# Kernel optimization log

Measured on AMD Instinct MI355X. Metric: run time of the kernel, lower is better.

The kernel has to match this reference:

```python
import jax, jax.numpy as jnp
import numpy as np

WS = 8        # window_size
OWIN = 12     # overlap_win_size = int(8*0.5)+8
PAD = 2       # (OWIN - WS)//2
HEADS = 4
DH = 16
INNER = HEADS * DH  # 64
DIM = 64


def _unfold(x, ws=WS, owin=OWIN, pad=PAD):
    # torch nn.Unfold(kernel=(owin,owin), stride=ws, padding=pad):
    # output [b, C*owin*owin, L] with channel ordering (c, kh, kw), L row-major over windows
    b, c, h, w = x.shape
    xp = jnp.pad(x, ((0, 0), (0, 0), (pad, pad), (pad, pad)))
    nH, nW = h // ws, w // ws
    ri = (jnp.arange(nH) * ws)[:, None] + jnp.arange(owin)[None, :]  # [nH, owin]
    ci = (jnp.arange(nW) * ws)[:, None] + jnp.arange(owin)[None, :]  # [nW, owin]
    p = xp[:, :, ri, :]          # [b, c, nH, owin, Wp]
    p = p[:, :, :, :, ci]        # [b, c, nH, owin, nW, owin]
    p = p.transpose(0, 1, 3, 5, 2, 4)  # [b, c, kh, kw, nH, nW]
    return p.reshape(b, c * owin * owin, nH * nW)


def setup_inputs() -> dict:
    key = jax.random.key(0)
    k1, k2, k3 = jax.random.split(key, 3)
    x = jax.random.normal(k1, (1, DIM, 64, 64), jnp.float32)
    w_qkv = jax.random.normal(k2, (3 * INNER, DIM), jnp.float32) * 0.05  # 1x1 conv, no bias
    w_out = jax.random.normal(k3, (DIM, INNER), jnp.float32) * 0.05     # 1x1 conv, no bias
    ln_w = jnp.ones((DIM,), jnp.float32)
    return {"x": x, "w_qkv": w_qkv, "w_out": w_out, "ln_w": ln_w}


def reference(x, w_qkv, w_out, ln_w):
    b, c, h, w = x.shape
    # BiasFree LayerNorm over channel dim (no mean subtraction)
    xc = x.transpose(0, 2, 3, 1)                       # b h w c
    var = jnp.var(xc, axis=-1, keepdims=True)
    xn = (xc / jnp.sqrt(var + 1e-5) * ln_w).transpose(0, 3, 1, 2)
    # qkv 1x1 conv
    qkv = jnp.einsum('bchw,oc->bohw', xn, w_qkv)
    qs, ks, vs = jnp.split(qkv, 3, axis=1)
    # queries: all h*w positions
    qs = qs.transpose(0, 2, 3, 1).reshape(b, h * w, HEADS, DH).transpose(0, 2, 1, 3)  # b heads N dh
    # keys/values: overlapping unfolded windows (faithful to torch reshape order)
    kk = _unfold(ks).reshape(b, INNER, -1).reshape(b, HEADS, -1, DH)  # b heads M dh
    vv = _unfold(vs).reshape(b, INNER, -1).reshape(b, HEADS, -1, DH)
    # rel_pos and fixed_mask are all-zero tensors in the source -> no-op bias
    attn = jnp.einsum('bhnd,bhmd->bhnm', qs, kk) * (DH ** -0.5)
    attn = jax.nn.softmax(attn, axis=-1)
    out = jnp.einsum('bhnm,bhmd->bhnd', attn, vv)
    out = out.transpose(0, 2, 1, 3).reshape(b, h, w, INNER).transpose(0, 3, 1, 2)
    return jnp.einsum('bchw,oc->bohw', out, w_out)
```

## Files before the change

### kernel.cpp

```cpp
#include <hip/hip_runtime.h>
#include <math.h>

#define PIX 4096
typedef unsigned short ushort_t;
typedef unsigned int uint_t;
typedef __attribute__((ext_vector_type(8))) short bf16x8;
typedef __attribute__((ext_vector_type(16))) float f32x16;

#define OFF_APART 524288
#define OFF_USHORT 2752512
#define U_QH 0
#define U_QL 262144
#define U_KF 524288
#define U_VF 1703936

#define QSCALE 0.36067376022224087f

#if defined(__has_builtin)
#if __has_builtin(__builtin_amdgcn_exp2f)
#define EXP2F(x) __builtin_amdgcn_exp2f(x)
#endif
#if __has_builtin(__builtin_amdgcn_perm)
#define PKHI16(u1, u0) __builtin_amdgcn_perm((u1), (u0), 0x07060302u)
#endif
#endif
#ifndef EXP2F
#define EXP2F(x) exp2f(x)
#endif
#ifndef PKHI16
#define PKHI16(u1, u0) (((u0) >> 16) | ((u1) & 0xFFFF0000u))
#endif

__device__ __forceinline__ void split_trunc(float x, ushort_t& hb, ushort_t& lb) {
    uint_t u = __float_as_uint(x);
    uint_t t = u & 0xFFFF0000u;
    float lo = x - __uint_as_float(t);
    hb = (ushort_t)(u >> 16);
    lb = (ushort_t)(__float_as_uint(lo) >> 16);
}

__device__ __forceinline__ void split8(const float* v, bf16x8& H, bf16x8& L) {
    union { uint_t u[4]; bf16x8 b; } hh, ll;
    #pragma unroll
    for (int j = 0; j < 4; ++j) {
        uint_t u0 = __float_as_uint(v[2 * j]), u1 = __float_as_uint(v[2 * j + 1]);
        hh.u[j] = PKHI16(u1, u0);
        float l0 = v[2 * j]     - __uint_as_float(u0 & 0xFFFF0000u);
        float l1 = v[2 * j + 1] - __uint_as_float(u1 & 0xFFFF0000u);
        ll.u[j] = PKHI16(__float_as_uint(l1), __float_as_uint(l0));
    }
    H = hh.b; L = ll.b;
}

__global__ __launch_bounds__(256)
void k_nq(const float* __restrict__ x, const float* __restrict__ w_qkv,
          const float* __restrict__ ln_w, float* __restrict__ qkvB,
          ushort_t* __restrict__ QH, ushort_t* __restrict__ QL)
{
    __shared__ float xs[64 * 32];
    __shared__ float red[2][8][32];
    __shared__ float rstd_s[32];
    __shared__ float lw[64];
    __shared__ ushort_t xh[32 * 64];
    __shared__ ushort_t xl[32 * 64];

    const int tid = threadIdx.x;
    const int px = tid & 31, cg = tid >> 5;
    const int pbase = ((int)blockIdx.x >> 1) * 32;
    const int ohalf = blockIdx.x & 1;

    if (tid < 64) lw[tid] = ln_w[tid];
    float s = 0.f, s2 = 0.f;
    #pragma unroll
    for (int cl = 0; cl < 8; ++cl) {
        int c = cg * 8 + cl;
        float v = x[c * PIX + pbase + px];
        xs[c * 32 + px] = v;
        s += v; s2 = fmaf(v, v, s2);
    }
    red[0][cg][px] = s; red[1][cg][px] = s2;
    __syncthreads();
    if (tid < 32) {
        float a = 0.f, b = 0.f;
        #pragma unroll
        for (int gidx = 0; gidx < 8; ++gidx) { a += red[0][gidx][tid]; b += red[1][gidx][tid]; }
        float mean = a * 0.015625f;
        float var  = fmaf(-mean, mean, b * 0.015625f);
        rstd_s[tid] = 1.0f / sqrtf(var + 1e-5f);
    }
    __syncthreads();
    {
        float vals[8];
        const float r = rstd_s[px];
        #pragma unroll
        for (int cl = 0; cl < 8; ++cl) {
            int c = cg * 8 + cl;
            vals[cl] = xs[c * 32 + px] * r * lw[c];
        }
        bf16x8 H, L; split8(vals, H, L);
        const int g = cg ^ (px & 7);
        *(bf16x8*)&xh[px * 64 + g * 8] = H;
        *(bf16x8*)&xl[px * 64 + g * 8] = L;
    }
    __syncthreads();

    const int w = tid >> 6;
    if (w >= 3) return;
    const int l = tid & 63, col = l & 31, rl = l >> 5;
    const int obase = ohalf * 96 + w * 32;

    bf16x8 wh[4], wl[4], xhf[4], xlf[4];
    const float* wrow = w_qkv + (obase + col) * 64;
    #pragma unroll
    for (int s4 = 0; s4 < 4; ++s4) {
        float tmp[8];
        *(float4*)&tmp[0] = *(const float4*)&wrow[s4 * 16 + rl * 8];
        *(float4*)&tmp[4] = *(const float4*)&wrow[s4 * 16 + rl * 8 + 4];
        split8(tmp, wh[s4], wl[s4]);
        const int g = (s4 * 2 + rl) ^ (col & 7);
        xhf[s4] = *(const bf16x8*)&xh[col * 64 + g * 8];
        xlf[s4] = *(const bf16x8*)&xl[col * 64 + g * 8];
    }
    f32x16 acc = {0,0,0,0,0,0,0,0,0,0,0,0,0,0,0,0};
    #pragma unroll
    for (int s4 = 0; s4 < 4; ++s4) {
        acc = __builtin_amdgcn_mfma_f32_32x32x16_bf16(wh[s4], xhf[s4], acc, 0, 0, 0);
        acc = __builtin_amdgcn_mfma_f32_32x32x16_bf16(wl[s4], xhf[s4], acc, 0, 0, 0);
        acc = __builtin_amdgcn_mfma_f32_32x32x16_bf16(wh[s4], xlf[s4], acc, 0, 0, 0);
    }
    const int gpx = pbase + col;
    #pragma unroll
    for (int j = 0; j < 16; ++j) {
        const int o = obase + (j & 3) + 8 * (j >> 2) + 4 * rl;
        if (o < 64) {
            float qv = acc[j] * QSCALE;
            ushort_t hb, lb; split_trunc(qv, hb, lb);
            const int a = ((o >> 4) * PIX + gpx) * 16 + (o & 15);
            QH[a] = hb; QL[a] = lb;
        } else {
            qkvB[(o - 64) * PIX + gpx] = acc[j];
        }
    }
}

__global__ __launch_bounds__(256)
void k_prep_kv(const float* __restrict__ qkvB,
               ushort_t* __restrict__ KF, ushort_t* __restrict__ VF)
{
    const int t = blockIdx.x * 256 + threadIdx.x;
    if (t < 589824) {
        int h = t / 147456; int r = t - h * 147456;
        int i = r >> 9; int r2 = r & 511;
        int l = r2 >> 3, j = r2 & 7;
        int col = l & 31, rl = l >> 5;
        int m = i * 32 + col;
        int d = rl * 8 + j;
        int cc = m / 576;  int r3 = m - cc * 576;
        int orr = r3 / 48; int r4 = r3 - orr * 48;
        int oc = r4 >> 2, wg = r4 & 3;
        int row  = wg * 16 + (d >> 3) * 8 + orr - 2;
        int colp = (d & 7) * 8 + oc - 2;
        bool ok = ((unsigned)row < 64u) && ((unsigned)colp < 64u);
        float v = ok ? qkvB[(h * 16 + cc) * PIX + row * 64 + colp] : 0.f;
        ushort_t hb, lb; split_trunc(v, hb, lb);
        int base = (h * 288 + i) * 1024 + l * 8 + j;
        KF[base] = hb; KF[base + 512] = lb;
    } else {
        int t2 = t - 589824;
        int h = t2 / 147456; int r = t2 - h * 147456;
        int i = r >> 9; int r2 = r & 511;
        int half = r2 >> 8; int r3 = r2 & 255;
        int rl = r3 >> 7; int colD = (r3 >> 3) & 15; int j2 = r3 & 7;
        int m = i * 32 + half * 16 + rl * 4 + (j2 & 3) + 8 * (j2 >> 2);
        int d = colD;
        int cc = m / 576;  int r4 = m - cc * 576;
        int orr = r4 / 48; int r5 = r4 - orr * 48;
        int oc = r5 >> 2, wg = r5 & 3;
        int row  = wg * 16 + (d >> 3) * 8 + orr - 2;
        int colp = (d & 7) * 8 + oc - 2;
        bool ok = ((unsigned)row < 64u) && ((unsigned)colp < 64u);
        float v = ok ? qkvB[(64 + h * 16 + cc) * PIX + row * 64 + colp] : 0.f;
        uint_t u = __float_as_uint(v);
        VF[(h * 288 + i) * 512 + half * 256 + (rl * 16 + colD) * 8 + j2] = (ushort_t)(u >> 16);
    }
}

__global__ __launch_bounds__(256)
void k_attn(const ushort_t* __restrict__ QH, const ushort_t* __restrict__ QL,
            const ushort_t* __restrict__ KF, const ushort_t* __restrict__ VF,
            float* __restrict__ APart)
{
    const int tid = threadIdx.x;
    const int w   = tid >> 6;
    const int l   = tid & 63;
    const int col = l & 31;
    const int rl  = l >> 5;

    const int bid  = blockIdx.x;
    const int x    = bid & 7;
    const int h    = x >> 1;
    const int tile = bid >> 3;
    const int ks   = (x & 1) * 4 + w;
    const int qbase = tile * 32;

    const bf16x8 qh = *(const bf16x8*)&QH[((h << 12) + qbase + col) * 16 + rl * 8];
    const bf16x8 ql = *(const bf16x8*)&QL[((h << 12) + qbase + col) * 16 + rl * 8];

    f32x16 acc = {0,0,0,0,0,0,0,0,0,0,0,0,0,0,0,0};
    const f32x16 zero = {0,0,0,0,0,0,0,0,0,0,0,0,0,0,0,0};

    union { uint_t u[4]; bf16x8 b; } vconst;
    const uint_t cfill = (col == 16) ? 0x3F803F80u : 0u;
    vconst.u[0] = cfill; vconst.u[1] = cfill; vconst.u[2] = cfill; vconst.u[3] = cfill;

    const ushort_t* kb = KF + (h * 288 + ks * 36) * 1024;
    const ushort_t* vb = VF + (h * 288 + ks * 36) * 512;

    bf16x8 kh = *(const bf16x8*)&kb[l * 8];
    bf16x8 kl = *(const bf16x8*)&kb[512 + l * 8];
    bf16x8 v0 = vconst.b, v1 = vconst.b;
    if (col < 16) {
        v0 = *(const bf16x8*)&vb[(rl * 16 + col) * 8];
        v1 = *(const bf16x8*)&vb[256 + (rl * 16 + col) * 8];
    }

    for (int i = 0; i < 36; ++i) {
        const bf16x8 ckh = kh, ckl = kl, cv0 = v0, cv1 = v1;
        if (i < 35) {
            kb += 1024; vb += 512;
            kh = *(const bf16x8*)&kb[l * 8];
            kl = *(const bf16x8*)&kb[512 + l * 8];
            if (col < 16) {
                v0 = *(const bf16x8*)&vb[(rl * 16 + col) * 8];
                v1 = *(const bf16x8*)&vb[256 + (rl * 16 + col) * 8];
            }
        }

        f32x16 S = __builtin_amdgcn_mfma_f32_32x32x16_bf16(ckh, qh, zero, 0, 0, 0);
        S = __builtin_amdgcn_mfma_f32_32x32x16_bf16(ckl, qh, S, 0, 0, 0);
        S = __builtin_amdgcn_mfma_f32_32x32x16_bf16(ckh, ql, S, 0, 0, 0);

        float p[16];
        #pragma unroll
        for (int r = 0; r < 16; ++r) p[r] = EXP2F(S[r]);

        union { uint_t u[4]; bf16x8 b; } A0, A1;
        #pragma unroll
        for (int j = 0; j < 4; ++j) {
            A0.u[j] = PKHI16(__float_as_uint(p[2 * j + 1]), __float_as_uint(p[2 * j]));
            A1.u[j] = PKHI16(__float_as_uint(p[8 + 2 * j + 1]), __float_as_uint(p[8 + 2 * j]));
        }
        acc = __builtin_amdgcn_mfma_f32_32x32x16_bf16(A0.b, cv0, acc, 0, 0, 0);
        acc = __builtin_amdgcn_mfma_f32_32x32x16_bf16(A1.b, cv1, acc, 0, 0, 0);
    }

    if (col <= 16) {
        float* base = APart + ((size_t)(ks * 4 + h) << 12) * 17;
        #pragma unroll
        for (int j = 0; j < 16; ++j) {
            const int q = qbase + (j & 3) + 8 * (j >> 2) + 4 * rl;
            base[q * 17 + col] = acc[j];
        }
    }
}

__global__ __launch_bounds__(256)
void k_proj(const float* __restrict__ APart, const float* __restrict__ w_out,
            float* __restrict__ out)
{
    __shared__ float asum[16 * 72];
    __shared__ float wo[64 * 68];
    __shared__ float as2[16 * 68];
    __shared__ float rdn[64];
    const int tid = threadIdx.x;
    const int pbase = blockIdx.x * 16;

    for (int idx = tid; idx < 1088; idx += 256) {
        int q_l = idx / 68; int rem = idx - q_l * 68;
        int h = rem / 17;  int c17 = rem - h * 17;
        float s = 0.f;
        #pragma unroll
        for (int ks = 0; ks < 8; ++ks)
            s += APart[((size_t)((ks * 4 + h) * PIX + pbase + q_l)) * 17 + c17];
        asum[q_l * 72 + h * 17 + c17] = s;
    }
    for (int idx = tid; idx < 4096; idx += 256)
        wo[(idx >> 6) * 68 + (idx & 63)] = w_out[idx];
    __syncthreads();
    if (tid < 64) {
        int h = tid >> 4, px = tid & 15;
        rdn[tid] = 1.0f / asum[px * 72 + h * 17 + 16];
    }
    __syncthreads();
    for (int idx = tid; idx < 1024; idx += 256) {
        int px = idx >> 6, ii = idx & 63;
        int h = ii >> 4, d = ii & 15;
        as2[px * 68 + ii] = asum[px * 72 + h * 17 + d] * rdn[h * 16 + px];
    }
    __syncthreads();

    const int pl = tid & 15;
    const int og = tid >> 4;
    float a0 = 0.f, a1 = 0.f, a2 = 0.f, a3 = 0.f;
    for (int c = 0; c < 64; c += 4) {
        const float4 xv = *(const float4*)&as2[pl * 68 + c];
        const float4 w0 = *(const float4*)&wo[(og * 4 + 0) * 68 + c];
        const float4 w1 = *(const float4*)&wo[(og * 4 + 1) * 68 + c];
        const float4 w2 = *(const float4*)&wo[(og * 4 + 2) * 68 + c];
        const float4 w3 = *(const float4*)&wo[(og * 4 + 3) * 68 + c];
        a0 = fmaf(xv.x, w0.x, fmaf(xv.y, w0.y, fmaf(xv.z, w0.z, fmaf(xv.w, w0.w, a0))));
        a1 = fmaf(xv.x, w1.x, fmaf(xv.y, w1.y, fmaf(xv.z, w1.z, fmaf(xv.w, w1.w, a1))));
        a2 = fmaf(xv.x, w2.x, fmaf(xv.y, w2.y, fmaf(xv.z, w2.z, fmaf(xv.w, w2.w, a2))));
        a3 = fmaf(xv.x, w3.x, fmaf(xv.y, w3.y, fmaf(xv.z, w3.z, fmaf(xv.w, w3.w, a3))));
    }
    out[(og * 4 + 0) * PIX + pbase + pl] = a0;
    out[(og * 4 + 1) * PIX + pbase + pl] = a1;
    out[(og * 4 + 2) * PIX + pbase + pl] = a2;
    out[(og * 4 + 3) * PIX + pbase + pl] = a3;
}

extern "C" void kernel_launch(void* const* d_in, const int* in_sizes, int n_in,
                              void* d_out, int out_size, void* d_ws, size_t ws_size,
                              hipStream_t stream)
{
    const float* x     = (const float*)d_in[0];
    const float* w_qkv = (const float*)d_in[1];
    const float* w_out = (const float*)d_in[2];
    const float* ln_w  = (const float*)d_in[3];
    float* out = (float*)d_out;
    float* ws  = (float*)d_ws;

    float* qkvB  = ws;
    float* APart = ws + OFF_APART;
    ushort_t* U  = (ushort_t*)(ws + OFF_USHORT);
    ushort_t* QH = U + U_QH;
    ushort_t* QL = U + U_QL;
    ushort_t* KF = U + U_KF;
    ushort_t* VF = U + U_VF;

    k_nq      <<<dim3(256),  dim3(256), 0, stream>>>(x, w_qkv, ln_w, qkvB, QH, QL);
    k_prep_kv <<<dim3(4608), dim3(256), 0, stream>>>(qkvB, KF, VF);
    k_attn    <<<dim3(1024), dim3(256), 0, stream>>>(QH, QL, KF, VF, APart);
    k_proj    <<<dim3(256),  dim3(256), 0, stream>>>(APart, w_out, out);
}
```

Before: 113.3 us.

## Process two query tiles per wave in attention and vectorize KV prep writes

Each attention wave now computes two 32-query tiles against the same K/V fragments. The block grows to 512 threads (8 key-split waves) and the grid shrinks to 256 blocks, so each K/V load is reused twice and the K/V traffic per query is halved. Separately, the KV prep kernel has each thread produce 8 packed bf16 values and write them as one 16-byte vector, replacing scalar ushort stores and cutting its grid size by a factor of eight. The cost is higher register pressure from two accumulators and two score tiles, plus fewer blocks, which may lower occupancy.

```diff
diff --git a/kernel.cpp b/kernel.cpp
--- a/kernel.cpp
+++ b/kernel.cpp
@@ -147,45 +147,57 @@
 void k_prep_kv(const float* __restrict__ qkvB,
                ushort_t* __restrict__ KF, ushort_t* __restrict__ VF)
 {
-    const int t = blockIdx.x * 256 + threadIdx.x;
-    if (t < 589824) {
-        int h = t / 147456; int r = t - h * 147456;
-        int i = r >> 9; int r2 = r & 511;
-        int l = r2 >> 3, j = r2 & 7;
-        int col = l & 31, rl = l >> 5;
-        int m = i * 32 + col;
-        int d = rl * 8 + j;
-        int cc = m / 576;  int r3 = m - cc * 576;
-        int orr = r3 / 48; int r4 = r3 - orr * 48;
-        int oc = r4 >> 2, wg = r4 & 3;
-        int row  = wg * 16 + (d >> 3) * 8 + orr - 2;
-        int colp = (d & 7) * 8 + oc - 2;
-        bool ok = ((unsigned)row < 64u) && ((unsigned)colp < 64u);
-        float v = ok ? qkvB[(h * 16 + cc) * PIX + row * 64 + colp] : 0.f;
-        ushort_t hb, lb; split_trunc(v, hb, lb);
-        int base = (h * 288 + i) * 1024 + l * 8 + j;
-        KF[base] = hb; KF[base + 512] = lb;
+    const int bid = blockIdx.x;
+    const int tid = threadIdx.x;
+    if (bid < 288) {
+        const int t = bid * 256 + tid;
+        const int h = t / 18432; int r = t - h * 18432;
+        const int i = r >> 6;   const int l = r & 63;
+        const int col = l & 31, rl = l >> 5;
+        const int m = i * 32 + col;
+        const int cc = m / 576;  const int r3 = m - cc * 576;
+        const int orr = r3 / 48; const int r4 = r3 - orr * 48;
+        const int oc = r4 >> 2, wg = r4 & 3;
+        const int row = wg * 16 + rl * 8 + orr - 2;
+        const bool rowOk = (unsigned)row < 64u;
+        const float* src = qkvB + (h * 16 + cc) * PIX + row * 64 + (oc - 2);
+        float vals[8];
+        #pragma unroll
+        for (int j = 0; j < 8; ++j) {
+            const int colp = j * 8 + oc - 2;
+            vals[j] = (rowOk && (unsigned)colp < 64u) ? src[j * 8] : 0.f;
+        }
+        bf16x8 H, L; split8(vals, H, L);
+        const int base = (h * 288 + i) * 1024 + l * 8;
+        *(bf16x8*)&KF[base]       = H;
+        *(bf16x8*)&KF[base + 512] = L;
     } else {
-        int t2 = t - 589824;
-        int h = t2 / 147456; int r = t2 - h * 147456;
-        int i = r >> 9; int r2 = r & 511;
-        int half = r2 >> 8; int r3 = r2 & 255;
-        int rl = r3 >> 7; int colD = (r3 >> 3) & 15; int j2 = r3 & 7;
-        int m = i * 32 + half * 16 + rl * 4 + (j2 & 3) + 8 * (j2 >> 2);
-        int d = colD;
-        int cc = m / 576;  int r4 = m - cc * 576;
-        int orr = r4 / 48; int r5 = r4 - orr * 48;
-        int oc = r5 >> 2, wg = r5 & 3;
-        int row  = wg * 16 + (d >> 3) * 8 + orr - 2;
-        int colp = (d & 7) * 8 + oc - 2;
-        bool ok = ((unsigned)row < 64u) && ((unsigned)colp < 64u);
-        float v = ok ? qkvB[(64 + h * 16 + cc) * PIX + row * 64 + colp] : 0.f;
-        uint_t u = __float_as_uint(v);
-        VF[(h * 288 + i) * 512 + half * 256 + (rl * 16 + colD) * 8 + j2] = (ushort_t)(u >> 16);
-    }
-}
-
-__global__ __launch_bounds__(256)
+        const int t = (bid - 288) * 256 + tid;
+        const int h = t / 18432; int r = t - h * 18432;
+        const int i = r >> 6;   const int r2 = r & 63;
+        const int half = r2 >> 5; const int rl = (r2 >> 4) & 1; const int colD = r2 & 15;
+        const int d = colD;
+        const int vcolp = (d & 7) * 8 - 2;
+        const int rbase = (d >> 3) * 8 - 2;
+        const float* srcp = qkvB + (64 + h * 16) * PIX;
+        union { ushort_t us[8]; bf16x8 b; } o8;
+        #pragma unroll
+        for (int j2 = 0; j2 < 8; ++j2) {
+            const int m = i * 32 + half * 16 + rl * 4 + (j2 & 3) + 8 * (j2 >> 2);
+            const int cc = m / 576;  const int r3 = m - cc * 576;
+            const int orr = r3 / 48; const int r4 = r3 - orr * 48;
+            const int oc = r4 >> 2, wg = r4 & 3;
+            const int row  = wg * 16 + rbase + orr;
+            const int colp = vcolp + oc;
+            const bool ok = ((unsigned)row < 64u) && ((unsigned)colp < 64u);
+            const float v = ok ? srcp[cc * PIX + row * 64 + colp] : 0.f;
+            o8.us[j2] = (ushort_t)(__float_as_uint(v) >> 16);
+        }
+        *(bf16x8*)&VF[(h * 288 + i) * 512 + half * 256 + (rl * 16 + colD) * 8] = o8.b;
+    }
+}
+
+__global__ __launch_bounds__(512)
 void k_attn(const ushort_t* __restrict__ QH, const ushort_t* __restrict__ QL,
             const ushort_t* __restrict__ KF, const ushort_t* __restrict__ VF,
             float* __restrict__ APart)
@@ -199,22 +211,26 @@
     const int bid  = blockIdx.x;
     const int x    = bid & 7;
     const int h    = x >> 1;
-    const int tile = bid >> 3;
-    const int ks   = (x & 1) * 4 + w;
-    const int qbase = tile * 32;
-
-    const bf16x8 qh = *(const bf16x8*)&QH[((h << 12) + qbase + col) * 16 + rl * 8];
-    const bf16x8 ql = *(const bf16x8*)&QL[((h << 12) + qbase + col) * 16 + rl * 8];
-
-    f32x16 acc = {0,0,0,0,0,0,0,0,0,0,0,0,0,0,0,0};
+    const int tile = ((bid >> 3) << 1) | (x & 1);
+    const int qbase = tile * 64;
+
+    const ushort_t* Qb = QH + ((h << 12) + qbase + col) * 16 + rl * 8;
+    const ushort_t* Qb2 = QL + ((h << 12) + qbase + col) * 16 + rl * 8;
+    const bf16x8 qh0 = *(const bf16x8*)&Qb[0];
+    const bf16x8 qh1 = *(const bf16x8*)&Qb[512];
+    const bf16x8 ql0 = *(const bf16x8*)&Qb2[0];
+    const bf16x8 ql1 = *(const bf16x8*)&Qb2[512];
+
+    f32x16 acc0 = {0,0,0,0,0,0,0,0,0,0,0,0,0,0,0,0};
+    f32x16 acc1 = {0,0,0,0,0,0,0,0,0,0,0,0,0,0,0,0};
     const f32x16 zero = {0,0,0,0,0,0,0,0,0,0,0,0,0,0,0,0};
 
     union { uint_t u[4]; bf16x8 b; } vconst;
     const uint_t cfill = (col == 16) ? 0x3F803F80u : 0u;
     vconst.u[0] = cfill; vconst.u[1] = cfill; vconst.u[2] = cfill; vconst.u[3] = cfill;
 
-    const ushort_t* kb = KF + (h * 288 + ks * 36) * 1024;
-    const ushort_t* vb = VF + (h * 288 + ks * 36) * 512;
+    const ushort_t* kb = KF + (h * 288 + w * 36) * 1024;
+    const ushort_t* vb = VF + (h * 288 + w * 36) * 512;
 
     bf16x8 kh = *(const bf16x8*)&kb[l * 8];
     bf16x8 kl = *(const bf16x8*)&kb[512 + l * 8];
@@ -236,30 +252,48 @@
             }
         }
 
-        f32x16 S = __builtin_amdgcn_mfma_f32_32x32x16_bf16(ckh, qh, zero, 0, 0, 0);
-        S = __builtin_amdgcn_mfma_f32_32x32x16_bf16(ckl, qh, S, 0, 0, 0);
-        S = __builtin_amdgcn_mfma_f32_32x32x16_bf16(ckh, ql, S, 0, 0, 0);
-
-        float p[16];
-        #pragma unroll
-        for (int r = 0; r < 16; ++r) p[r] = EXP2F(S[r]);
-
-        union { uint_t u[4]; bf16x8 b; } A0, A1;
-        #pragma unroll
-        for (int j = 0; j < 4; ++j) {
-            A0.u[j] = PKHI16(__float_as_uint(p[2 * j + 1]), __float_as_uint(p[2 * j]));
-            A1.u[j] = PKHI16(__float_as_uint(p[8 + 2 * j + 1]), __float_as_uint(p[8 + 2 * j]));
-        }
-        acc = __builtin_amdgcn_mfma_f32_32x32x16_bf16(A0.b, cv0, acc, 0, 0, 0);
-        acc = __builtin_amdgcn_mfma_f32_32x32x16_bf16(A1.b, cv1, acc, 0, 0, 0);
+        f32x16 S0 = __builtin_amdgcn_mfma_f32_32x32x16_bf16(ckh, qh0, zero, 0, 0, 0);
+        S0 = __builtin_amdgcn_mfma_f32_32x32x16_bf16(ckl, qh0, S0, 0, 0, 0);
+        S0 = __builtin_amdgcn_mfma_f32_32x32x16_bf16(ckh, ql0, S0, 0, 0, 0);
+        f32x16 S1 = __builtin_amdgcn_mfma_f32_32x32x16_bf16(ckh, qh1, zero, 0, 0, 0);
+        S1 = __builtin_amdgcn_mfma_f32_32x32x16_bf16(ckl, qh1, S1, 0, 0, 0);
+        S1 = __builtin_amdgcn_mfma_f32_32x32x16_bf16(ckh, ql1, S1, 0, 0, 0);
+
+        {
+            float p[16];
+            #pragma unroll
+            for (int r = 0; r < 16; ++r) p[r] = EXP2F(S0[r]);
+            union { uint_t u[4]; bf16x8 b; } A0, A1;
+            #pragma unroll
+            for (int j = 0; j < 4; ++j) {
+                A0.u[j] = PKHI16(__float_as_uint(p[2 * j + 1]), __float_as_uint(p[2 * j]));
+                A1.u[j] = PKHI16(__float_as_uint(p[8 + 2 * j + 1]), __float_as_uint(p[8 + 2 * j]));
+            }
+            acc0 = __builtin_amdgcn_mfma_f32_32x32x16_bf16(A0.b, cv0, acc0, 0, 0, 0);
+            acc0 = __builtin_amdgcn_mfma_f32_32x32x16_bf16(A1.b, cv1, acc0, 0, 0, 0);
+        }
+        {
+            float p[16];
+            #pragma unroll
+            for (int r = 0; r < 16; ++r) p[r] = EXP2F(S1[r]);
+            union { uint_t u[4]; bf16x8 b; } A0, A1;
+            #pragma unroll
+            for (int j = 0; j < 4; ++j) {
+                A0.u[j] = PKHI16(__float_as_uint(p[2 * j + 1]), __float_as_uint(p[2 * j]));
+                A1.u[j] = PKHI16(__float_as_uint(p[8 + 2 * j + 1]), __float_as_uint(p[8 + 2 * j]));
+            }
+            acc1 = __builtin_amdgcn_mfma_f32_32x32x16_bf16(A0.b, cv0, acc1, 0, 0, 0);
+            acc1 = __builtin_amdgcn_mfma_f32_32x32x16_bf16(A1.b, cv1, acc1, 0, 0, 0);
+        }
     }
 
     if (col <= 16) {
-        float* base = APart + ((size_t)(ks * 4 + h) << 12) * 17;
+        float* base = APart + ((size_t)(w * 4 + h) << 12) * 17;
         #pragma unroll
         for (int j = 0; j < 16; ++j) {
             const int q = qbase + (j & 3) + 8 * (j >> 2) + 4 * rl;
-            base[q * 17 + col] = acc[j];
+            base[q * 17 + col]        = acc0[j];
+            base[(q + 32) * 17 + col] = acc1[j];
         }
     }
 }
@@ -338,8 +372,8 @@
     ushort_t* KF = U + U_KF;
     ushort_t* VF = U + U_VF;
 
-    k_nq      <<<dim3(256),  dim3(256), 0, stream>>>(x, w_qkv, ln_w, qkvB, QH, QL);
-    k_prep_kv <<<dim3(4608), dim3(256), 0, stream>>>(qkvB, KF, VF);
-    k_attn    <<<dim3(1024), dim3(256), 0, stream>>>(QH, QL, KF, VF, APart);
-    k_proj    <<<dim3(256),  dim3(256), 0, stream>>>(APart, w_out, out);
-}
+    k_nq      <<<dim3(256), dim3(256), 0, stream>>>(x, w_qkv, ln_w, qkvB, QH, QL);
+    k_prep_kv <<<dim3(576), dim3(256), 0, stream>>>(qkvB, KF, VF);
+    k_attn    <<<dim3(256), dim3(512), 0, stream>>>(QH, QL, KF, VF, APart);
+    k_proj    <<<dim3(256), dim3(256), 0, stream>>>(APart, w_out, out);
+}
```

New measurement: 104.7 us. 1.08x faster.
